# Performance work log

Measured on AMD Instinct MI355X. Metric: run time of the kernel, lower is better.

The kernel has to match this reference:

```python
import jax, jax.numpy as jnp
import numpy as np

B, S, E = 256, 512, 768          # batch, seq_len, embed_dim (= 2*hidden_dim)
MD = 2 * 384 + 1                 # memory feature dim after location column = 769
HOPS, OUT = 3, 3


def setup_inputs() -> dict:
    key = jax.random.key(0)
    ks = jax.random.split(key, 9)
    memory = jax.random.normal(ks[0], (B, S, E), dtype=jnp.float32)
    aspect = jax.random.normal(ks[1], (B, E), dtype=jnp.float32)
    att_w = jax.random.normal(ks[2], (MD + 2 * E,), dtype=jnp.float32) * 0.02
    att_b = jnp.zeros((1,), dtype=jnp.float32)
    gru_w_ih = jax.random.normal(ks[3], (3 * E, MD), dtype=jnp.float32) * 0.02
    gru_w_hh = jax.random.normal(ks[4], (3 * E, E), dtype=jnp.float32) * 0.02
    gru_b_ih = jnp.zeros((3 * E,), dtype=jnp.float32)
    gru_b_hh = jnp.zeros((3 * E,), dtype=jnp.float32)
    dense_w = jax.random.normal(ks[5], (E, OUT), dtype=jnp.float32) * 0.02
    dense_b = jnp.zeros((OUT,), dtype=jnp.float32)
    memory_len = jax.random.randint(ks[6], (B,), S // 2, S + 1, dtype=jnp.int32)
    left_len = jax.random.randint(ks[7], (B,), 0, 64, dtype=jnp.int32)
    aspect_len = jax.random.randint(ks[8], (B,), 1, 8, dtype=jnp.int32)
    return dict(memory=memory, aspect=aspect, att_w=att_w, att_b=att_b,
                gru_w_ih=gru_w_ih, gru_w_hh=gru_w_hh, gru_b_ih=gru_b_ih,
                gru_b_hh=gru_b_hh, dense_w=dense_w, dense_b=dense_b,
                memory_len=memory_len, left_len=left_len, aspect_len=aspect_len,
                hops=HOPS)


def _locationed_memory(memory, memory_len, left_len, aspect_len):
    # Vectorized form of the nested python loop: per-position location-decay
    # weight and signed-offset column u, only for idx < memory_len.
    dt = memory.dtype
    idx = jnp.arange(memory.shape[1], dtype=jnp.int32)[None, :]   # [1,S]
    start = left_len[:, None]
    alen = aspect_len[:, None]
    mlen = memory_len[:, None]
    before = idx < start
    after_off = idx - start - alen + 1
    u = jnp.where(before, idx - start,
                  jnp.where(idx < start + alen, 0, after_off)).astype(dt)
    l = jnp.where(before, start - idx,
                  jnp.where(idx < start + alen, 0, after_off)).astype(dt)
    valid = idx < mlen
    w = jnp.where(valid, 1.0 - l / mlen.astype(dt), 1.0)
    u = jnp.where(valid, u, 0.0)
    mem = memory * w[:, :, None]
    return jnp.concatenate([mem, u[:, :, None]], axis=-1)        # [B,S,MD]


def _gru_cell(x, h, w_ih, w_hh, b_ih, b_hh):
    gi = x @ w_ih.T + b_ih
    gh = h @ w_hh.T + b_hh
    ir, iz, in_ = jnp.split(gi, 3, axis=-1)
    hr, hz, hn = jnp.split(gh, 3, axis=-1)
    r = jax.nn.sigmoid(ir + hr)
    z = jax.nn.sigmoid(iz + hz)
    n = jnp.tanh(in_ + r * hn)
    return (1.0 - z) * n + z * h


def reference(memory, aspect, att_w, att_b, gru_w_ih, gru_w_hh, gru_b_ih,
              gru_b_hh, dense_w, dense_b, memory_len, left_len, aspect_len,
              hops):
    mem = _locationed_memory(memory, memory_len, left_len, aspect_len)
    # att_linear(cat([mem, et, aspect])) split into three small matvecs
    w_mem = att_w[:MD]
    w_et = att_w[MD:MD + E]
    w_asp = att_w[MD + E:]
    g_static = mem @ w_mem + (aspect @ w_asp)[:, None] + att_b[0]  # [B,S]
    et = jnp.zeros_like(aspect)
    for _ in range(hops):
        g = g_static + (et @ w_et)[:, None]                        # [B,S]
        alpha = jax.nn.softmax(g, axis=1)
        i = jnp.einsum('bs,bsd->bd', alpha, mem)                   # [B,MD]
        et = _gru_cell(i, et, gru_w_ih, gru_w_hh, gru_b_ih, gru_b_hh)
    logits = et @ dense_w + dense_b                                # [B,OUT]
    return logits
```

## Files before the change

kernel.cpp:

```cpp
#include <hip/hip_runtime.h>
#include <math.h>

#define Bn 256
#define Sn 512
#define En 768
#define G3n 2304
#define TAIL_BLOCKS 192
#define GRP 24

typedef __attribute__((ext_vector_type(8))) short short8;
typedef __attribute__((ext_vector_type(4))) float f32x4;

__device__ __forceinline__ float sigmoidf_(float x) { return 1.f / (1.f + __expf(-x)); }
__device__ __forceinline__ float tanhf_(float x) {
  float e = __expf(2.f * x);
  return (e - 1.f) / (e + 1.f);
}

__device__ __forceinline__ unsigned short f2bf(float x) {
  unsigned int u = __builtin_bit_cast(unsigned int, x);
  u += 0x7FFFu + ((u >> 16) & 1u);
  return (unsigned short)(u >> 16);
}
__device__ __forceinline__ float bf2f(unsigned short u) {
  unsigned int x = ((unsigned int)u) << 16;
  return __builtin_bit_cast(float, x);
}

__device__ __forceinline__ void loc_uw(int s, int start, int al, int ml, float& u, float& w) {
  float uu;
  if (s < start)            uu = (float)(s - start);
  else if (s < start + al)  uu = 0.f;
  else                      uu = (float)(s - start - al + 1);
  float l = fabsf(uu);
  if (s < ml) { w = 1.f - l / (float)ml; u = uu; }
  else        { w = 1.f; u = 0.f; }
}

__device__ __forceinline__ void group_barrier(unsigned int* cnt, unsigned int expected) {
  __syncthreads();
  if (threadIdx.x == 0) {
    __threadfence();
    __hip_atomic_fetch_add(cnt, 1u, __ATOMIC_ACQ_REL, __HIP_MEMORY_SCOPE_AGENT);
    while (__hip_atomic_load(cnt, __ATOMIC_ACQUIRE, __HIP_MEMORY_SCOPE_AGENT) < expected)
      __builtin_amdgcn_s_sleep(2);
    __threadfence();
  }
  __syncthreads();
}

__global__ __launch_bounds__(1024) void k_mega(
    const float* __restrict__ mem, const float* __restrict__ att_w,
    const int* __restrict__ mlen, const int* __restrict__ llen, const int* __restrict__ alen,
    const float* __restrict__ w_ih, const float* __restrict__ w_hh,
    float* __restrict__ pacc, float* __restrict__ pm,
    float* __restrict__ pz, float* __restrict__ piu,
    unsigned short* __restrict__ wi_bf, unsigned short* __restrict__ wh_bf,
    const float* __restrict__ db, float* __restrict__ out,
    unsigned int* __restrict__ barcnt) {
  __shared__ float accL[16][En];
  __shared__ float mL[16], zL[16], iuL[16];
  int bc = blockIdx.x;
  int tid = threadIdx.x;

  if (bc >= 512) {
    int cb = bc - 512;
    int mat = cb >= 216;
    int t = (cb - mat * 216) * 1024 + tid;
    int idx = t * 8;
    int r = idx / En, c = idx - r * En;
    const float* src;
    unsigned short* dst;
    if (mat == 0) { src = w_ih + (size_t)r * 769 + c; dst = wi_bf + idx; }
    else          { src = w_hh + (size_t)r * En  + c; dst = wh_bf + idx; }
    unsigned int p[4];
#pragma unroll
    for (int j = 0; j < 4; ++j) {
      unsigned int lo = f2bf(src[2 * j]);
      unsigned int hi = f2bf(src[2 * j + 1]);
      p[j] = lo | (hi << 16);
    }
    *reinterpret_cast<uint4*>(dst) = make_uint4(p[0], p[1], p[2], p[3]);
    if (bc == 512) {
      if (tid < 768)                 out[tid] = db[tid % 3];
      else if (tid < 768 + 16)       barcnt[tid - 768] = 0u;
    }
    return;
  }

  int b = bc >> 1, half = bc & 1;
  int wv = tid >> 6, lane = tid & 63;

  float4 w0 = *reinterpret_cast<const float4*>(att_w + lane * 4);
  float4 w1 = *reinterpret_cast<const float4*>(att_w + 256 + lane * 4);
  float4 w2 = *reinterpret_cast<const float4*>(att_w + 512 + lane * 4);
  float wtail = att_w[En];
  int start = llen[b], al = alen[b], ml = mlen[b];
  int s0row = half * 256 + wv * 16;
  const float* base = mem + ((size_t)b * Sn + s0row) * En;

  float m = -1e30f, z = 0.f, iu = 0.f;
  float4 a0 = {0, 0, 0, 0}, a1 = {0, 0, 0, 0}, a2 = {0, 0, 0, 0};
  float4 v0 = *reinterpret_cast<const float4*>(base + lane * 4);
  float4 v1 = *reinterpret_cast<const float4*>(base + 256 + lane * 4);
  float4 v2 = *reinterpret_cast<const float4*>(base + 512 + lane * 4);

  for (int r = 0; r < 16; ++r) {
    float4 c0 = v0, c1 = v1, c2 = v2;
    if (r < 15) {
      const float* nrow = base + (size_t)(r + 1) * En;
      v0 = *reinterpret_cast<const float4*>(nrow + lane * 4);
      v1 = *reinterpret_cast<const float4*>(nrow + 256 + lane * 4);
      v2 = *reinterpret_cast<const float4*>(nrow + 512 + lane * 4);
    }
    float dot = c0.x * w0.x + c0.y * w0.y + c0.z * w0.z + c0.w * w0.w
              + c1.x * w1.x + c1.y * w1.y + c1.z * w1.z + c1.w * w1.w
              + c2.x * w2.x + c2.y * w2.y + c2.z * w2.z + c2.w * w2.w;
#pragma unroll
    for (int off = 32; off; off >>= 1) dot += __shfl_xor(dot, off);
    int s = s0row + r;
    float u, w;
    loc_uw(s, start, al, ml, u, w);
    float g = w * dot + u * wtail;
    if (g > m) {
      float f = __expf(m - g);
      z *= f; iu *= f;
      a0.x *= f; a0.y *= f; a0.z *= f; a0.w *= f;
      a1.x *= f; a1.y *= f; a1.z *= f; a1.w *= f;
      a2.x *= f; a2.y *= f; a2.z *= f; a2.w *= f;
      m = g;
    }
    float e = __expf(g - m);
    z += e; iu += e * u;
    float sc = e * w;
    a0.x += sc * c0.x; a0.y += sc * c0.y; a0.z += sc * c0.z; a0.w += sc * c0.w;
    a1.x += sc * c1.x; a1.y += sc * c1.y; a1.z += sc * c1.z; a1.w += sc * c1.w;
    a2.x += sc * c2.x; a2.y += sc * c2.y; a2.z += sc * c2.z; a2.w += sc * c2.w;
  }

  *reinterpret_cast<float4*>(&accL[wv][lane * 4])       = a0;
  *reinterpret_cast<float4*>(&accL[wv][256 + lane * 4]) = a1;
  *reinterpret_cast<float4*>(&accL[wv][512 + lane * 4]) = a2;
  if (lane == 0) { mL[wv] = m; zL[wv] = z; iuL[wv] = iu; }
  __syncthreads();

  float M = mL[0];
#pragma unroll
  for (int i = 1; i < 16; ++i) M = fmaxf(M, mL[i]);
  float f[16], Z = 0.f, IU = 0.f;
#pragma unroll
  for (int i = 0; i < 16; ++i) {
    f[i] = __expf(mL[i] - M);
    Z += zL[i] * f[i];
    IU += iuL[i] * f[i];
  }
  if (tid < En) {
    float s = 0.f;
#pragma unroll
    for (int i = 0; i < 16; ++i) s += f[i] * accL[i][tid];
    pacc[(size_t)bc * En + tid] = s;
  }
  if (tid == 0) { pm[bc] = M; pz[bc] = Z; piu[bc] = IU; }
}

__global__ __launch_bounds__(512) void k_tail(
    const float* __restrict__ pacc, const float* __restrict__ pm,
    const float* __restrict__ pz, const float* __restrict__ piu,
    const unsigned short* __restrict__ wi_bf, const unsigned short* __restrict__ wh_bf,
    const float* __restrict__ w_ih, const float* __restrict__ b_ih,
    const float* __restrict__ b_hh, float* __restrict__ gi,
    unsigned short* __restrict__ eta_bf, unsigned short* __restrict__ etb_bf,
    const float* __restrict__ dw, float* __restrict__ out,
    unsigned int* __restrict__ barcnt) {
  __shared__ unsigned short As[32][264];
  __shared__ unsigned short Bs[3][32][264];
  __shared__ float red[4][64][17];
  __shared__ float rowF0[32], rowF1[32], rowAu[32];
  int bid = blockIdx.x;
  int mgrp = bid / GRP;
  int e0 = (bid - mgrp * GRP) * 32, m0 = mgrp * 32;
  int tid = threadIdx.x;
  int lane = tid & 63, wv = tid >> 6;
  int p = wv & 3, kh = wv >> 2;
  int wm = p >> 1, we = p & 1;
  int l15 = lane & 15, l4 = lane >> 4;

  if (tid < 32) {
    int m = m0 + tid;
    float ma = pm[2 * m], mb = pm[2 * m + 1];
    float M = fmaxf(ma, mb);
    float f0 = __expf(ma - M), f1 = __expf(mb - M);
    float iv = 1.f / (pz[2 * m] * f0 + pz[2 * m + 1] * f1);
    rowF0[tid] = f0 * iv;
    rowF1[tid] = f1 * iv;
    rowAu[tid] = (piu[2 * m] * f0 + piu[2 * m + 1] * f1) * iv;
  }

  for (int hop = 0; hop < 3; ++hop) {
    const unsigned short* Wbf = (hop == 0) ? wi_bf : wh_bf;
    const unsigned short* Abf = (hop == 1) ? eta_bf : etb_bf;

    f32x4 acc[3];
#pragma unroll
    for (int g = 0; g < 3; ++g) { acc[g][0] = 0.f; acc[g][1] = 0.f; acc[g][2] = 0.f; acc[g][3] = 0.f; }

    for (int kb = 0; kb < 3; ++kb) {
      int kbase = kb * 256;
      __syncthreads();
      if (hop == 0) {
#pragma unroll
        for (int i = 0; i < 2; ++i) {
          int idx = tid + i * 512;
          int row = idx >> 5, ch = idx & 31;
          float f0 = rowF0[row], f1 = rowF1[row];
          const float* q0 = pacc + (size_t)(2 * (m0 + row)) * En + kbase + ch * 8;
          const float* q1 = q0 + En;
          float4 x0 = *reinterpret_cast<const float4*>(q0);
          float4 x1 = *reinterpret_cast<const float4*>(q0 + 4);
          float4 y0 = *reinterpret_cast<const float4*>(q1);
          float4 y1 = *reinterpret_cast<const float4*>(q1 + 4);
          unsigned int pk[4];
          pk[0] = (unsigned int)f2bf(f0 * x0.x + f1 * y0.x)
                | ((unsigned int)f2bf(f0 * x0.y + f1 * y0.y) << 16);
          pk[1] = (unsigned int)f2bf(f0 * x0.z + f1 * y0.z)
                | ((unsigned int)f2bf(f0 * x0.w + f1 * y0.w) << 16);
          pk[2] = (unsigned int)f2bf(f0 * x1.x + f1 * y1.x)
                | ((unsigned int)f2bf(f0 * x1.y + f1 * y1.y) << 16);
          pk[3] = (unsigned int)f2bf(f0 * x1.z + f1 * y1.z)
                | ((unsigned int)f2bf(f0 * x1.w + f1 * y1.w) << 16);
          *reinterpret_cast<uint4*>(&As[row][ch * 8]) = make_uint4(pk[0], pk[1], pk[2], pk[3]);
        }
      } else {
#pragma unroll
        for (int i = 0; i < 2; ++i) {
          int idx = tid + i * 512;
          int row = idx >> 5, ch = idx & 31;
          *reinterpret_cast<uint4*>(&As[row][ch * 8]) =
              *reinterpret_cast<const uint4*>(Abf + (size_t)(m0 + row) * En + kbase + ch * 8);
        }
      }
#pragma unroll
      for (int i = 0; i < 6; ++i) {
        int idx = tid + i * 512;
        int g = idx >> 10, rem = idx & 1023;
        int row = rem >> 5, ch = rem & 31;
        *reinterpret_cast<uint4*>(&Bs[g][row][ch * 8]) =
            *reinterpret_cast<const uint4*>(Wbf + (size_t)(g * En + e0 + row) * En + kbase + ch * 8);
      }
      __syncthreads();
#pragma unroll
      for (int ks = 0; ks < 4; ++ks) {
        int col = kh * 128 + ks * 32 + l4 * 8;
        short8 a = *reinterpret_cast<const short8*>(&As[wm * 16 + l15][col]);
#pragma unroll
        for (int g = 0; g < 3; ++g) {
          short8 bfr = *reinterpret_cast<const short8*>(&Bs[g][we * 16 + l15][col]);
          acc[g] = __builtin_amdgcn_mfma_f32_16x16x32_bf16(a, bfr, acc[g], 0, 0, 0);
        }
      }
    }

    __syncthreads();
    if (kh == 1) {
#pragma unroll
      for (int g = 0; g < 3; ++g)
#pragma unroll
        for (int j = 0; j < 4; ++j) red[p][lane][g * 4 + j] = acc[g][j];
    }
    __syncthreads();
    if (kh == 0) {
#pragma unroll
      for (int g = 0; g < 3; ++g)
#pragma unroll
        for (int j = 0; j < 4; ++j) acc[g][j] += red[p][lane][g * 4 + j];

      int ecol = e0 + we * 16 + l15;
      int mbase = m0 + wm * 16 + l4 * 4;
      float bhr = b_hh[ecol], bhz = b_hh[En + ecol], bhn = b_hh[2 * En + ecol];
      float vout[4];
      if (hop == 0) {
        float wn0 = w_ih[(size_t)ecol * 769 + En];
        float wn1 = w_ih[(size_t)(En + ecol) * 769 + En];
        float wn2 = w_ih[(size_t)(2 * En + ecol) * 769 + En];
        float bi0 = b_ih[ecol], bi1 = b_ih[En + ecol], bi2 = b_ih[2 * En + ecol];
#pragma unroll
        for (int j = 0; j < 4; ++j) {
          int m = mbase + j;
          float au = rowAu[wm * 16 + l4 * 4 + j];
          float gr = acc[0][j] + au * wn0 + bi0;
          float gz = acc[1][j] + au * wn1 + bi1;
          float gn = acc[2][j] + au * wn2 + bi2;
          gi[(size_t)m * G3n + ecol]          = gr;
          gi[(size_t)m * G3n + En + ecol]     = gz;
          gi[(size_t)m * G3n + 2 * En + ecol] = gn;
          float r = sigmoidf_(gr + bhr);
          float z = sigmoidf_(gz + bhz);
          float n = tanhf_(gn + r * bhn);
          vout[j] = (1.f - z) * n;
          eta_bf[(size_t)m * En + ecol] = f2bf(vout[j]);
        }
      } else {
#pragma unroll
        for (int j = 0; j < 4; ++j) {
          int m = mbase + j;
          float rr = sigmoidf_(gi[(size_t)m * G3n + ecol] + acc[0][j] + bhr);
          float zz = sigmoidf_(gi[(size_t)m * G3n + En + ecol] + acc[1][j] + bhz);
          float nn = tanhf_(gi[(size_t)m * G3n + 2 * En + ecol] + rr * (acc[2][j] + bhn));
          float h = bf2f(Abf[(size_t)m * En + ecol]);
          vout[j] = (1.f - zz) * nn + zz * h;
        }
        if (hop == 1) {
#pragma unroll
          for (int j = 0; j < 4; ++j)
            etb_bf[(size_t)(mbase + j) * En + ecol] = f2bf(vout[j]);
        } else {
          float dw0 = dw[ecol * 3 + 0], dw1 = dw[ecol * 3 + 1], dw2 = dw[ecol * 3 + 2];
          float pp[4][3];
#pragma unroll
          for (int j = 0; j < 4; ++j) {
            pp[j][0] = vout[j] * dw0;
            pp[j][1] = vout[j] * dw1;
            pp[j][2] = vout[j] * dw2;
          }
#pragma unroll
          for (int off = 1; off < 16; off <<= 1)
#pragma unroll
            for (int j = 0; j < 4; ++j) {
              pp[j][0] += __shfl_xor(pp[j][0], off);
              pp[j][1] += __shfl_xor(pp[j][1], off);
              pp[j][2] += __shfl_xor(pp[j][2], off);
            }
          if (l15 == 0) {
#pragma unroll
            for (int j = 0; j < 4; ++j) {
              atomicAdd(&out[(mbase + j) * 3 + 0], pp[j][0]);
              atomicAdd(&out[(mbase + j) * 3 + 1], pp[j][1]);
              atomicAdd(&out[(mbase + j) * 3 + 2], pp[j][2]);
            }
          }
        }
      }
    }
    if (hop < 2) group_barrier(&barcnt[hop * 8 + mgrp], GRP);
  }
}

extern "C" void kernel_launch(void* const* d_in, const int* in_sizes, int n_in,
                              void* d_out, int out_size, void* d_ws, size_t ws_size,
                              hipStream_t stream) {
  const float* memory   = (const float*)d_in[0];
  const float* att_w    = (const float*)d_in[2];
  const float* gru_w_ih = (const float*)d_in[4];
  const float* gru_w_hh = (const float*)d_in[5];
  const float* gru_b_ih = (const float*)d_in[6];
  const float* gru_b_hh = (const float*)d_in[7];
  const float* dense_w  = (const float*)d_in[8];
  const float* dense_b  = (const float*)d_in[9];
  const int* memory_len = (const int*)d_in[10];
  const int* left_len   = (const int*)d_in[11];
  const int* aspect_len = (const int*)d_in[12];
  float* out = (float*)d_out;

  unsigned short* wi_bf  = (unsigned short*)d_ws;
  unsigned short* wh_bf  = wi_bf + (size_t)G3n * En;
  unsigned short* eta_bf = wh_bf + (size_t)G3n * En;
  unsigned short* etb_bf = eta_bf + (size_t)Bn * En;
  float* pm     = (float*)(etb_bf + (size_t)Bn * En);
  float* pz     = pm + 2 * Bn;
  float* piu    = pz + 2 * Bn;
  float* pacc   = piu + 2 * Bn;
  float* gi     = pacc + (size_t)2 * Bn * En;
  unsigned int* barcnt = (unsigned int*)(gi + (size_t)Bn * G3n);

  k_mega<<<dim3(944), 1024, 0, stream>>>(memory, att_w, memory_len, left_len, aspect_len,
                                         gru_w_ih, gru_w_hh, pacc, pm, pz, piu, wi_bf, wh_bf,
                                         dense_b, out, barcnt);
  k_tail<<<dim3(TAIL_BLOCKS), 512, 0, stream>>>(pacc, pm, pz, piu, wi_bf, wh_bf,
                                                gru_w_ih, gru_b_ih, gru_b_hh, gi,
                                                eta_bf, etb_bf, dense_w, out, barcnt);
}
```

Before: 138.6 us.

## Replace persistent tail with atomic group barriers by three per-hop kernel launches

The single persistent tail kernel, which used spin-wait atomic group barriers between GRU hops, is split into three templated kernel launches, one per hop, with a 2D grid. Shared memory is overlaid so the reduction buffer reuses the B-tile region, and the barrier counter reset is removed. This trades the in-kernel software barrier for two extra kernel launches and their launch gaps.

```diff
diff --git a/kernel.cpp b/kernel.cpp
--- a/kernel.cpp
+++ b/kernel.cpp
@@ -5,8 +5,6 @@
 #define Sn 512
 #define En 768
 #define G3n 2304
-#define TAIL_BLOCKS 192
-#define GRP 24
 
 typedef __attribute__((ext_vector_type(8))) short short8;
 typedef __attribute__((ext_vector_type(4))) float f32x4;
@@ -37,18 +35,6 @@
   else        { w = 1.f; u = 0.f; }
 }
 
-__device__ __forceinline__ void group_barrier(unsigned int* cnt, unsigned int expected) {
-  __syncthreads();
-  if (threadIdx.x == 0) {
-    __threadfence();
-    __hip_atomic_fetch_add(cnt, 1u, __ATOMIC_ACQ_REL, __HIP_MEMORY_SCOPE_AGENT);
-    while (__hip_atomic_load(cnt, __ATOMIC_ACQUIRE, __HIP_MEMORY_SCOPE_AGENT) < expected)
-      __builtin_amdgcn_s_sleep(2);
-    __threadfence();
-  }
-  __syncthreads();
-}
-
 __global__ __launch_bounds__(1024) void k_mega(
     const float* __restrict__ mem, const float* __restrict__ att_w,
     const int* __restrict__ mlen, const int* __restrict__ llen, const int* __restrict__ alen,
@@ -56,8 +42,7 @@
     float* __restrict__ pacc, float* __restrict__ pm,
     float* __restrict__ pz, float* __restrict__ piu,
     unsigned short* __restrict__ wi_bf, unsigned short* __restrict__ wh_bf,
-    const float* __restrict__ db, float* __restrict__ out,
-    unsigned int* __restrict__ barcnt) {
+    const float* __restrict__ db, float* __restrict__ out) {
   __shared__ float accL[16][En];
   __shared__ float mL[16], zL[16], iuL[16];
   int bc = blockIdx.x;
@@ -81,10 +66,7 @@
       p[j] = lo | (hi << 16);
     }
     *reinterpret_cast<uint4*>(dst) = make_uint4(p[0], p[1], p[2], p[3]);
-    if (bc == 512) {
-      if (tid < 768)                 out[tid] = db[tid % 3];
-      else if (tid < 768 + 16)       barcnt[tid - 768] = 0u;
-    }
+    if (bc == 512 && tid < 768) out[tid] = db[tid % 3];
     return;
   }
 
@@ -163,29 +145,29 @@
   if (tid == 0) { pm[bc] = M; pz[bc] = Z; piu[bc] = IU; }
 }
 
-__global__ __launch_bounds__(512) void k_tail(
+template <int MODE>
+__global__ __launch_bounds__(512) void k_fused(
     const float* __restrict__ pacc, const float* __restrict__ pm,
     const float* __restrict__ pz, const float* __restrict__ piu,
-    const unsigned short* __restrict__ wi_bf, const unsigned short* __restrict__ wh_bf,
+    const unsigned short* __restrict__ Abf, const unsigned short* __restrict__ Wbf,
     const float* __restrict__ w_ih, const float* __restrict__ b_ih,
     const float* __restrict__ b_hh, float* __restrict__ gi,
-    unsigned short* __restrict__ eta_bf, unsigned short* __restrict__ etb_bf,
-    const float* __restrict__ dw, float* __restrict__ out,
-    unsigned int* __restrict__ barcnt) {
-  __shared__ unsigned short As[32][264];
-  __shared__ unsigned short Bs[3][32][264];
-  __shared__ float red[4][64][17];
+    unsigned short* __restrict__ et_out_bf,
+    const float* __restrict__ dw, float* __restrict__ out) {
+  __shared__ __align__(16) unsigned char lds[16896 + 50688];
+  auto As = reinterpret_cast<unsigned short(*)[264]>(lds);
+  auto Bs = reinterpret_cast<unsigned short(*)[32][264]>(lds + 16896);
+  float* red = reinterpret_cast<float*>(lds + 16896);
   __shared__ float rowF0[32], rowF1[32], rowAu[32];
-  int bid = blockIdx.x;
-  int mgrp = bid / GRP;
-  int e0 = (bid - mgrp * GRP) * 32, m0 = mgrp * 32;
+
+  int e0 = blockIdx.x * 32, m0 = blockIdx.y * 32;
   int tid = threadIdx.x;
   int lane = tid & 63, wv = tid >> 6;
   int p = wv & 3, kh = wv >> 2;
   int wm = p >> 1, we = p & 1;
   int l15 = lane & 15, l4 = lane >> 4;
 
-  if (tid < 32) {
+  if (MODE == 0 && tid < 32) {
     int m = m0 + tid;
     float ma = pm[2 * m], mb = pm[2 * m + 1];
     float M = fmaxf(ma, mb);
@@ -196,152 +178,145 @@
     rowAu[tid] = (piu[2 * m] * f0 + piu[2 * m + 1] * f1) * iv;
   }
 
-  for (int hop = 0; hop < 3; ++hop) {
-    const unsigned short* Wbf = (hop == 0) ? wi_bf : wh_bf;
-    const unsigned short* Abf = (hop == 1) ? eta_bf : etb_bf;
-
-    f32x4 acc[3];
-#pragma unroll
-    for (int g = 0; g < 3; ++g) { acc[g][0] = 0.f; acc[g][1] = 0.f; acc[g][2] = 0.f; acc[g][3] = 0.f; }
-
-    for (int kb = 0; kb < 3; ++kb) {
-      int kbase = kb * 256;
-      __syncthreads();
-      if (hop == 0) {
-#pragma unroll
-        for (int i = 0; i < 2; ++i) {
-          int idx = tid + i * 512;
-          int row = idx >> 5, ch = idx & 31;
-          float f0 = rowF0[row], f1 = rowF1[row];
-          const float* q0 = pacc + (size_t)(2 * (m0 + row)) * En + kbase + ch * 8;
-          const float* q1 = q0 + En;
-          float4 x0 = *reinterpret_cast<const float4*>(q0);
-          float4 x1 = *reinterpret_cast<const float4*>(q0 + 4);
-          float4 y0 = *reinterpret_cast<const float4*>(q1);
-          float4 y1 = *reinterpret_cast<const float4*>(q1 + 4);
-          unsigned int pk[4];
-          pk[0] = (unsigned int)f2bf(f0 * x0.x + f1 * y0.x)
-                | ((unsigned int)f2bf(f0 * x0.y + f1 * y0.y) << 16);
-          pk[1] = (unsigned int)f2bf(f0 * x0.z + f1 * y0.z)
-                | ((unsigned int)f2bf(f0 * x0.w + f1 * y0.w) << 16);
-          pk[2] = (unsigned int)f2bf(f0 * x1.x + f1 * y1.x)
-                | ((unsigned int)f2bf(f0 * x1.y + f1 * y1.y) << 16);
-          pk[3] = (unsigned int)f2bf(f0 * x1.z + f1 * y1.z)
-                | ((unsigned int)f2bf(f0 * x1.w + f1 * y1.w) << 16);
-          *reinterpret_cast<uint4*>(&As[row][ch * 8]) = make_uint4(pk[0], pk[1], pk[2], pk[3]);
-        }
-      } else {
-#pragma unroll
-        for (int i = 0; i < 2; ++i) {
-          int idx = tid + i * 512;
-          int row = idx >> 5, ch = idx & 31;
-          *reinterpret_cast<uint4*>(&As[row][ch * 8]) =
-              *reinterpret_cast<const uint4*>(Abf + (size_t)(m0 + row) * En + kbase + ch * 8);
-        }
-      }
-#pragma unroll
-      for (int i = 0; i < 6; ++i) {
+  f32x4 acc[3];
+#pragma unroll
+  for (int g = 0; g < 3; ++g) { acc[g][0] = 0.f; acc[g][1] = 0.f; acc[g][2] = 0.f; acc[g][3] = 0.f; }
+
+  for (int kb = 0; kb < 3; ++kb) {
+    int kbase = kb * 256;
+    __syncthreads();
+    if (MODE == 0) {
+#pragma unroll
+      for (int i = 0; i < 2; ++i) {
         int idx = tid + i * 512;
-        int g = idx >> 10, rem = idx & 1023;
-        int row = rem >> 5, ch = rem & 31;
-        *reinterpret_cast<uint4*>(&Bs[g][row][ch * 8]) =
-            *reinterpret_cast<const uint4*>(Wbf + (size_t)(g * En + e0 + row) * En + kbase + ch * 8);
-      }
-      __syncthreads();
-#pragma unroll
-      for (int ks = 0; ks < 4; ++ks) {
-        int col = kh * 128 + ks * 32 + l4 * 8;
-        short8 a = *reinterpret_cast<const short8*>(&As[wm * 16 + l15][col]);
-#pragma unroll
-        for (int g = 0; g < 3; ++g) {
-          short8 bfr = *reinterpret_cast<const short8*>(&Bs[g][we * 16 + l15][col]);
-          acc[g] = __builtin_amdgcn_mfma_f32_16x16x32_bf16(a, bfr, acc[g], 0, 0, 0);
-        }
-      }
-    }
-
+        int row = idx >> 5, ch = idx & 31;
+        float f0 = rowF0[row], f1 = rowF1[row];
+        const float* q0 = pacc + (size_t)(2 * (m0 + row)) * En + kbase + ch * 8;
+        const float* q1 = q0 + En;
+        float4 x0 = *reinterpret_cast<const float4*>(q0);
+        float4 x1 = *reinterpret_cast<const float4*>(q0 + 4);
+        float4 y0 = *reinterpret_cast<const float4*>(q1);
+        float4 y1 = *reinterpret_cast<const float4*>(q1 + 4);
+        unsigned int pk[4];
+        pk[0] = (unsigned int)f2bf(f0 * x0.x + f1 * y0.x)
+              | ((unsigned int)f2bf(f0 * x0.y + f1 * y0.y) << 16);
+        pk[1] = (unsigned int)f2bf(f0 * x0.z + f1 * y0.z)
+              | ((unsigned int)f2bf(f0 * x0.w + f1 * y0.w) << 16);
+        pk[2] = (unsigned int)f2bf(f0 * x1.x + f1 * y1.x)
+              | ((unsigned int)f2bf(f0 * x1.y + f1 * y1.y) << 16);
+        pk[3] = (unsigned int)f2bf(f0 * x1.z + f1 * y1.z)
+              | ((unsigned int)f2bf(f0 * x1.w + f1 * y1.w) << 16);
+        *reinterpret_cast<uint4*>(&As[row][ch * 8]) = make_uint4(pk[0], pk[1], pk[2], pk[3]);
+      }
+    } else {
+#pragma unroll
+      for (int i = 0; i < 2; ++i) {
+        int idx = tid + i * 512;
+        int row = idx >> 5, ch = idx & 31;
+        *reinterpret_cast<uint4*>(&As[row][ch * 8]) =
+            *reinterpret_cast<const uint4*>(Abf + (size_t)(m0 + row) * En + kbase + ch * 8);
+      }
+    }
+#pragma unroll
+    for (int i = 0; i < 6; ++i) {
+      int idx = tid + i * 512;
+      int g = idx >> 10, rem = idx & 1023;
+      int row = rem >> 5, ch = rem & 31;
+      *reinterpret_cast<uint4*>(&Bs[g][row][ch * 8]) =
+          *reinterpret_cast<const uint4*>(Wbf + (size_t)(g * En + e0 + row) * En + kbase + ch * 8);
+    }
     __syncthreads();
-    if (kh == 1) {
-#pragma unroll
-      for (int g = 0; g < 3; ++g)
-#pragma unroll
-        for (int j = 0; j < 4; ++j) red[p][lane][g * 4 + j] = acc[g][j];
-    }
-    __syncthreads();
-    if (kh == 0) {
-#pragma unroll
-      for (int g = 0; g < 3; ++g)
-#pragma unroll
-        for (int j = 0; j < 4; ++j) acc[g][j] += red[p][lane][g * 4 + j];
-
-      int ecol = e0 + we * 16 + l15;
-      int mbase = m0 + wm * 16 + l4 * 4;
-      float bhr = b_hh[ecol], bhz = b_hh[En + ecol], bhn = b_hh[2 * En + ecol];
-      float vout[4];
-      if (hop == 0) {
-        float wn0 = w_ih[(size_t)ecol * 769 + En];
-        float wn1 = w_ih[(size_t)(En + ecol) * 769 + En];
-        float wn2 = w_ih[(size_t)(2 * En + ecol) * 769 + En];
-        float bi0 = b_ih[ecol], bi1 = b_ih[En + ecol], bi2 = b_ih[2 * En + ecol];
-#pragma unroll
-        for (int j = 0; j < 4; ++j) {
-          int m = mbase + j;
-          float au = rowAu[wm * 16 + l4 * 4 + j];
-          float gr = acc[0][j] + au * wn0 + bi0;
-          float gz = acc[1][j] + au * wn1 + bi1;
-          float gn = acc[2][j] + au * wn2 + bi2;
-          gi[(size_t)m * G3n + ecol]          = gr;
-          gi[(size_t)m * G3n + En + ecol]     = gz;
-          gi[(size_t)m * G3n + 2 * En + ecol] = gn;
-          float r = sigmoidf_(gr + bhr);
-          float z = sigmoidf_(gz + bhz);
-          float n = tanhf_(gn + r * bhn);
-          vout[j] = (1.f - z) * n;
-          eta_bf[(size_t)m * En + ecol] = f2bf(vout[j]);
-        }
-      } else {
-#pragma unroll
-        for (int j = 0; j < 4; ++j) {
-          int m = mbase + j;
-          float rr = sigmoidf_(gi[(size_t)m * G3n + ecol] + acc[0][j] + bhr);
-          float zz = sigmoidf_(gi[(size_t)m * G3n + En + ecol] + acc[1][j] + bhz);
-          float nn = tanhf_(gi[(size_t)m * G3n + 2 * En + ecol] + rr * (acc[2][j] + bhn));
-          float h = bf2f(Abf[(size_t)m * En + ecol]);
-          vout[j] = (1.f - zz) * nn + zz * h;
-        }
-        if (hop == 1) {
-#pragma unroll
-          for (int j = 0; j < 4; ++j)
-            etb_bf[(size_t)(mbase + j) * En + ecol] = f2bf(vout[j]);
-        } else {
-          float dw0 = dw[ecol * 3 + 0], dw1 = dw[ecol * 3 + 1], dw2 = dw[ecol * 3 + 2];
-          float pp[4][3];
-#pragma unroll
-          for (int j = 0; j < 4; ++j) {
-            pp[j][0] = vout[j] * dw0;
-            pp[j][1] = vout[j] * dw1;
-            pp[j][2] = vout[j] * dw2;
-          }
-#pragma unroll
-          for (int off = 1; off < 16; off <<= 1)
-#pragma unroll
-            for (int j = 0; j < 4; ++j) {
-              pp[j][0] += __shfl_xor(pp[j][0], off);
-              pp[j][1] += __shfl_xor(pp[j][1], off);
-              pp[j][2] += __shfl_xor(pp[j][2], off);
-            }
-          if (l15 == 0) {
-#pragma unroll
-            for (int j = 0; j < 4; ++j) {
-              atomicAdd(&out[(mbase + j) * 3 + 0], pp[j][0]);
-              atomicAdd(&out[(mbase + j) * 3 + 1], pp[j][1]);
-              atomicAdd(&out[(mbase + j) * 3 + 2], pp[j][2]);
-            }
-          }
-        }
-      }
-    }
-    if (hop < 2) group_barrier(&barcnt[hop * 8 + mgrp], GRP);
+#pragma unroll
+    for (int ks = 0; ks < 4; ++ks) {
+      int col = kh * 128 + ks * 32 + l4 * 8;
+      short8 a = *reinterpret_cast<const short8*>(&As[wm * 16 + l15][col]);
+#pragma unroll
+      for (int g = 0; g < 3; ++g) {
+        short8 bfr = *reinterpret_cast<const short8*>(&Bs[g][we * 16 + l15][col]);
+        acc[g] = __builtin_amdgcn_mfma_f32_16x16x32_bf16(a, bfr, acc[g], 0, 0, 0);
+      }
+    }
+  }
+
+  __syncthreads();
+  if (kh == 1) {
+#pragma unroll
+    for (int g = 0; g < 3; ++g)
+#pragma unroll
+      for (int j = 0; j < 4; ++j) red[(p * 64 + lane) * 17 + g * 4 + j] = acc[g][j];
+  }
+  __syncthreads();
+  if (kh == 1) return;
+#pragma unroll
+  for (int g = 0; g < 3; ++g)
+#pragma unroll
+    for (int j = 0; j < 4; ++j) acc[g][j] += red[(p * 64 + lane) * 17 + g * 4 + j];
+
+  int ecol = e0 + we * 16 + l15;
+  int mbase = m0 + wm * 16 + l4 * 4;
+  float bhr = b_hh[ecol], bhz = b_hh[En + ecol], bhn = b_hh[2 * En + ecol];
+  float vout[4];
+  if (MODE == 0) {
+    float wn0 = w_ih[(size_t)ecol * 769 + En];
+    float wn1 = w_ih[(size_t)(En + ecol) * 769 + En];
+    float wn2 = w_ih[(size_t)(2 * En + ecol) * 769 + En];
+    float bi0 = b_ih[ecol], bi1 = b_ih[En + ecol], bi2 = b_ih[2 * En + ecol];
+#pragma unroll
+    for (int j = 0; j < 4; ++j) {
+      int m = mbase + j;
+      float au = rowAu[wm * 16 + l4 * 4 + j];
+      float gr = acc[0][j] + au * wn0 + bi0;
+      float gz = acc[1][j] + au * wn1 + bi1;
+      float gn = acc[2][j] + au * wn2 + bi2;
+      gi[(size_t)m * G3n + ecol]          = gr;
+      gi[(size_t)m * G3n + En + ecol]     = gz;
+      gi[(size_t)m * G3n + 2 * En + ecol] = gn;
+      float r = sigmoidf_(gr + bhr);
+      float z = sigmoidf_(gz + bhz);
+      float n = tanhf_(gn + r * bhn);
+      vout[j] = (1.f - z) * n;
+    }
+  } else {
+#pragma unroll
+    for (int j = 0; j < 4; ++j) {
+      int m = mbase + j;
+      float rr = sigmoidf_(gi[(size_t)m * G3n + ecol] + acc[0][j] + bhr);
+      float zz = sigmoidf_(gi[(size_t)m * G3n + En + ecol] + acc[1][j] + bhz);
+      float nn = tanhf_(gi[(size_t)m * G3n + 2 * En + ecol] + rr * (acc[2][j] + bhn));
+      float h = bf2f(Abf[(size_t)m * En + ecol]);
+      vout[j] = (1.f - zz) * nn + zz * h;
+    }
+  }
+
+  if (MODE != 2) {
+#pragma unroll
+    for (int j = 0; j < 4; ++j)
+      et_out_bf[(size_t)(mbase + j) * En + ecol] = f2bf(vout[j]);
+  } else {
+    float dw0 = dw[ecol * 3 + 0], dw1 = dw[ecol * 3 + 1], dw2 = dw[ecol * 3 + 2];
+    float pp[4][3];
+#pragma unroll
+    for (int j = 0; j < 4; ++j) {
+      pp[j][0] = vout[j] * dw0;
+      pp[j][1] = vout[j] * dw1;
+      pp[j][2] = vout[j] * dw2;
+    }
+#pragma unroll
+    for (int off = 1; off < 16; off <<= 1)
+#pragma unroll
+      for (int j = 0; j < 4; ++j) {
+        pp[j][0] += __shfl_xor(pp[j][0], off);
+        pp[j][1] += __shfl_xor(pp[j][1], off);
+        pp[j][2] += __shfl_xor(pp[j][2], off);
+      }
+    if (l15 == 0) {
+#pragma unroll
+      for (int j = 0; j < 4; ++j) {
+        atomicAdd(&out[(mbase + j) * 3 + 0], pp[j][0]);
+        atomicAdd(&out[(mbase + j) * 3 + 1], pp[j][1]);
+        atomicAdd(&out[(mbase + j) * 3 + 2], pp[j][2]);
+      }
+    }
   }
 }
 
@@ -370,12 +345,17 @@
   float* piu    = pz + 2 * Bn;
   float* pacc   = piu + 2 * Bn;
   float* gi     = pacc + (size_t)2 * Bn * En;
-  unsigned int* barcnt = (unsigned int*)(gi + (size_t)Bn * G3n);
 
   k_mega<<<dim3(944), 1024, 0, stream>>>(memory, att_w, memory_len, left_len, aspect_len,
                                          gru_w_ih, gru_w_hh, pacc, pm, pz, piu, wi_bf, wh_bf,
-                                         dense_b, out, barcnt);
-  k_tail<<<dim3(TAIL_BLOCKS), 512, 0, stream>>>(pacc, pm, pz, piu, wi_bf, wh_bf,
-                                                gru_w_ih, gru_b_ih, gru_b_hh, gi,
-                                                eta_bf, etb_bf, dense_w, out, barcnt);
-}
+                                         dense_b, out);
+  k_fused<0><<<dim3(En / 32, Bn / 32), 512, 0, stream>>>(
+      pacc, pm, pz, piu, nullptr, wi_bf, gru_w_ih, gru_b_ih, gru_b_hh, gi, eta_bf,
+      nullptr, nullptr);
+  k_fused<1><<<dim3(En / 32, Bn / 32), 512, 0, stream>>>(
+      nullptr, nullptr, nullptr, nullptr, eta_bf, wh_bf, nullptr, nullptr, gru_b_hh, gi, etb_bf,
+      nullptr, nullptr);
+  k_fused<2><<<dim3(En / 32, Bn / 32), 512, 0, stream>>>(
+      nullptr, nullptr, nullptr, nullptr, etb_bf, wh_bf, nullptr, nullptr, gru_b_hh, gi, nullptr,
+      dense_w, out);
+}
```

New measurement: 116.6 us, median of 3. 1.19x faster.
